# Performance work log

Measured on AMD Instinct MI355X. Metric: run time of the kernel, lower is better.

Reference implementation:

```python
import jax, jax.numpy as jnp
import numpy as np

DIM = 1024
NUM_HEADS = 16
HEAD_DIM = DIM // NUM_HEADS
SCALING = HEAD_DIM ** (-0.5)


def setup_inputs() -> dict:
    key = jax.random.key(0)
    ks = jax.random.split(key, 9)
    B, S = 2, 2048
    s = DIM ** -0.5  # ~ torch Linear init scale
    inp = {
        "x": jax.random.normal(ks[0], (B, S, DIM), dtype=jnp.float32),
        "wq": jax.random.uniform(ks[1], (DIM, DIM), jnp.float32, -s, s),
        "bq": jax.random.uniform(ks[2], (DIM,), jnp.float32, -s, s),
        "wk": jax.random.uniform(ks[3], (DIM, DIM), jnp.float32, -s, s),
        "bk": jax.random.uniform(ks[4], (DIM,), jnp.float32, -s, s),
        "wv": jax.random.uniform(ks[5], (DIM, DIM), jnp.float32, -s, s),
        "bv": jax.random.uniform(ks[6], (DIM,), jnp.float32, -s, s),
        "wo": jax.random.uniform(ks[7], (DIM, DIM), jnp.float32, -s, s),
        "bo": jax.random.uniform(ks[8], (DIM,), jnp.float32, -s, s),
    }
    return inp


def reference(x, wq, bq, wk, bk, wv, bv, wo, bo):
    B, S, D = x.shape
    # projections (weights stored [out,in] like torch Linear -> x @ W.T + b)
    q = (x @ wq.T + bq).reshape(B, S, NUM_HEADS, HEAD_DIM)
    k = (x @ wk.T + bk).reshape(B, S, NUM_HEADS, HEAD_DIM)
    v = (x @ wv.T + bv).reshape(B, S, NUM_HEADS, HEAD_DIM)
    # [B,H,S,S] scores, scaled
    scores = jnp.einsum("bqhd,bkhd->bhqk", q, k) * SCALING
    attn = jax.nn.softmax(scores, axis=-1)
    # dropout p=0.0 (eval): identity
    out = jnp.einsum("bhqk,bkhd->bqhd", attn, v).reshape(B, S, D)
    return out @ wo.T + bo
```

## Files before the change

kernel.cpp:

```cpp
#include <hip/hip_runtime.h>

#define DIM 1024
#define NHEADS 16
#define HDIM 64
#define BATCH 2
#define SEQ 2048
#define MTOT (BATCH*SEQ)
#define QSCALE 0.18033688011112042f
#define XN ((size_t)MTOT*DIM)
#define WN ((size_t)DIM*DIM)

typedef __attribute__((ext_vector_type(8))) short short8;
typedef __attribute__((ext_vector_type(4))) float f32x4;
typedef __attribute__((ext_vector_type(16))) float f32x16;
typedef __attribute__((ext_vector_type(2))) int int2v;

static __device__ __forceinline__ unsigned short bf16rne(float f) {
    unsigned u = __builtin_bit_cast(unsigned, f);
    return (unsigned short)((u + 0x7fffu + ((u >> 16) & 1u)) >> 16);
}

static __device__ __forceinline__ void gld16(const void* g, void* l) {
    __builtin_amdgcn_global_load_lds((const __attribute__((address_space(1))) void*)g,
                                     (__attribute__((address_space(3))) void*)l, 16, 0, 0);
}

static __device__ __forceinline__ f32x16 mfma32(short8 a, short8 b, f32x16 c) {
    return __builtin_amdgcn_mfma_f32_32x32x16_bf16(a, b, c, 0, 0, 0);
}

__global__ __launch_bounds__(256)
void prep(const float* __restrict__ x, const float* __restrict__ wq, const float* __restrict__ wk,
          const float* __restrict__ wv, const float* __restrict__ wo, unsigned short* __restrict__ dst)
{
    const size_t i = ((size_t)blockIdx.x*256 + threadIdx.x)*8;
    const float* s; size_t o;
    if (i < XN)           { s = x;  o = i; }
    else if (i < XN+WN)   { s = wq; o = i - XN; }
    else if (i < XN+2*WN) { s = wk; o = i - XN - WN; }
    else if (i < XN+3*WN) { s = wv; o = i - XN - 2*WN; }
    else                  { s = wo; o = i - XN - 3*WN; }
    float4 a = *(const float4*)(s + o);
    float4 b = *(const float4*)(s + o + 4);
    uint4 w;
    w.x = (unsigned)bf16rne(a.x) | ((unsigned)bf16rne(a.y) << 16);
    w.y = (unsigned)bf16rne(a.z) | ((unsigned)bf16rne(a.w) << 16);
    w.z = (unsigned)bf16rne(b.x) | ((unsigned)bf16rne(b.y) << 16);
    w.w = (unsigned)bf16rne(b.z) | ((unsigned)bf16rne(b.w) << 16);
    *(uint4*)&dst[i] = w;
}

__global__ __launch_bounds__(256)
void gemm_qkv(const unsigned short* __restrict__ A,
              const unsigned short* __restrict__ W0, const unsigned short* __restrict__ W1,
              const unsigned short* __restrict__ W2,
              const float* __restrict__ b0, const float* __restrict__ b1, const float* __restrict__ b2,
              unsigned short* __restrict__ o0, unsigned short* __restrict__ o1, unsigned short* __restrict__ o2)
{
    __shared__ __align__(16) unsigned short smem[24576];
    #define AS(s) (smem + (s)*4096)
    #define BS(s) (smem + 12288 + (s)*4096)
    const int t = threadIdx.x, wid = t >> 6, lane = t & 63;
    const int lr = lane & 15, lg = lane >> 4;
    const int bid = blockIdx.y * 24 + blockIdx.x;
    const int swz = (bid & 7) * 96 + (bid >> 3);
    const int sx = swz % 24, sy = swz / 24;
    const int widx = sx >> 3;
    const int n0 = (sx & 7) << 7;
    const int m0 = sy << 7;
    const unsigned short* W = widx == 0 ? W0 : (widx == 1 ? W1 : W2);
    const float* bias        = widx == 0 ? b0 : (widx == 1 ? b1 : b2);

    const int wm = wid >> 1, wn = wid & 1;
    const int f0 = 2*wid, f1 = f0 + 1;
    const unsigned short* Ag0 = A + (size_t)(m0 + f0*16 + lr)*DIM + lg*8;
    const unsigned short* Ag1 = A + (size_t)(m0 + f1*16 + lr)*DIM + lg*8;
    const unsigned short* Bg0 = W + (size_t)(n0 + f0*16 + lr)*DIM + lg*8;
    const unsigned short* Bg1 = W + (size_t)(n0 + f1*16 + lr)*DIM + lg*8;

    auto stage = [&](int tt, int slot) {
        const int ko = tt * 32;
        gld16(Ag0 + ko, AS(slot) + f0*512); gld16(Ag1 + ko, AS(slot) + f1*512);
        gld16(Bg0 + ko, BS(slot) + f0*512); gld16(Bg1 + ko, BS(slot) + f1*512);
    };

    f32x4 acc[4][4] = {};
    stage(0, 0); stage(1, 1);
    int c0 = 0, c1 = 1, c2 = 2;

    for (int it = 0; it < DIM/32; ++it) {
        if (it < DIM/32 - 2) { asm volatile("s_waitcnt vmcnt(4)" ::: "memory"); }
        else                 { asm volatile("s_waitcnt vmcnt(0)" ::: "memory"); }
        __builtin_amdgcn_s_barrier();
        short8 af[4], bf[4];
        #pragma unroll
        for (int i = 0; i < 4; ++i) af[i] = *(const short8*)(AS(c0) + (wm*4+i)*512 + lane*8);
        #pragma unroll
        for (int i = 0; i < 4; ++i) bf[i] = *(const short8*)(BS(c0) + (wn*4+i)*512 + lane*8);
        if (it + 2 < DIM/32) stage(it + 2, c2);
        __builtin_amdgcn_s_setprio(1);
        #pragma unroll
        for (int mb = 0; mb < 4; ++mb)
            #pragma unroll
            for (int nb = 0; nb < 4; ++nb)
                acc[mb][nb] = __builtin_amdgcn_mfma_f32_16x16x32_bf16(af[mb], bf[nb], acc[mb][nb], 0, 0, 0);
        __builtin_amdgcn_s_setprio(0);
        const int tmp = c0; c0 = c1; c1 = c2; c2 = tmp;
    }

    if (widx == 0) {
        #pragma unroll
        for (int nb = 0; nb < 4; ++nb) {
            const int col = n0 + wn*64 + nb*16 + lr;
            const float bv = bias[col];
            #pragma unroll
            for (int mb = 0; mb < 4; ++mb) {
                #pragma unroll
                for (int j = 0; j < 4; ++j) {
                    const int row = m0 + wm*64 + mb*16 + lg*4 + j;
                    o0[(size_t)row*DIM + col] = bf16rne((acc[mb][nb][j] + bv) * QSCALE);
                }
            }
        }
    } else {
        unsigned short* outp = (widx == 1) ? o1 : o2;
        const int isV = (widx == 2);
        __syncthreads();
        unsigned short (*tile)[136] = (unsigned short (*)[136])smem;
        #pragma unroll
        for (int nb = 0; nb < 4; ++nb) {
            const int col = wn*64 + nb*16 + lr;
            const float bv = bias[n0 + col];
            #pragma unroll
            for (int mb = 0; mb < 4; ++mb) {
                #pragma unroll
                for (int j = 0; j < 4; ++j)
                    tile[wm*64 + mb*16 + lg*4 + j][col] = bf16rne(acc[mb][nb][j] + bv);
            }
        }
        __syncthreads();
        const int bb  = m0 >> 11;
        const int kt0 = (m0 & (SEQ-1)) >> 6;
        const int hh0 = n0 >> 6;
        #pragma unroll
        for (int shot = 0; shot < 8; ++shot) {
            const int idx = t + shot*256;
            const int tid = idx >> 9;
            const int fr  = (idx >> 6) & 7;
            const int ln  = idx & 63;
            const int ktl = tid & 1, hhl = tid >> 1;
            short8 ov;
            if (isV) {
                const int r0 = ktl*64 + (fr & 3)*16 + (ln >> 5)*8;
                const int c  = hhl*64 + (fr >> 2)*32 + (ln & 31);
                #pragma unroll
                for (int e = 0; e < 8; ++e) ov[e] = (short)tile[r0 + e][c];
            } else {
                const int r  = ktl*64 + (fr >> 2)*32 + (ln & 31);
                const int cc = hhl*64 + (fr & 3)*16 + (ln >> 5)*8;
                ov = *(const short8*)&tile[r][cc];
            }
            unsigned short* dst = outp
                + ((size_t)((bb*NHEADS + hh0 + hhl)*32 + kt0 + ktl))*4096 + fr*512 + ln*8;
            *(short8*)dst = ov;
        }
    }
    #undef AS
    #undef BS
}

__global__ __launch_bounds__(256)
void gemm_o(const unsigned short* __restrict__ A, const unsigned short* __restrict__ W,
            const float* __restrict__ bias, float* __restrict__ fo)
{
    __shared__ __align__(16) unsigned short As[3][2048];
    __shared__ __align__(16) unsigned short Bs[3][4096];
    const int t = threadIdx.x, wid = t >> 6, lane = t & 63;
    const int lr = lane & 15, lg = lane >> 4;
    const int bid = blockIdx.y * 8 + blockIdx.x;
    const int swz = (bid & 7) * 64 + (bid >> 3);
    const int n0 = (swz & 7) << 7;
    const int m0 = (swz >> 3) << 6;
    const int wm = wid >> 1, wn = wid & 1;

    const int fa = wid;
    const int g0 = 2*wid, g1 = g0 + 1;
    const unsigned short* Ag  = A + (size_t)(m0 + fa*16 + lr)*DIM + lg*8;
    const unsigned short* Bg0 = W + (size_t)(n0 + g0*16 + lr)*DIM + lg*8;
    const unsigned short* Bg1 = W + (size_t)(n0 + g1*16 + lr)*DIM + lg*8;

    auto stage = [&](int tt, int slot) {
        const int ko = tt * 32;
        gld16(Ag + ko, &As[slot][fa*512]);
        gld16(Bg0 + ko, &Bs[slot][g0*512]); gld16(Bg1 + ko, &Bs[slot][g1*512]);
    };

    f32x4 acc[2][4] = {};
    stage(0, 0); stage(1, 1);
    int c0 = 0, c1 = 1, c2 = 2;

    for (int it = 0; it < DIM/32; ++it) {
        if (it < DIM/32 - 2) { asm volatile("s_waitcnt vmcnt(3)" ::: "memory"); }
        else                 { asm volatile("s_waitcnt vmcnt(0)" ::: "memory"); }
        __builtin_amdgcn_s_barrier();
        short8 af[2], bf[4];
        #pragma unroll
        for (int i = 0; i < 2; ++i) af[i] = *(const short8*)&As[c0][(wm*2+i)*512 + lane*8];
        #pragma unroll
        for (int i = 0; i < 4; ++i) bf[i] = *(const short8*)&Bs[c0][(wn*4+i)*512 + lane*8];
        if (it + 2 < DIM/32) stage(it + 2, c2);
        __builtin_amdgcn_s_setprio(1);
        #pragma unroll
        for (int mb = 0; mb < 2; ++mb)
            #pragma unroll
            for (int nb = 0; nb < 4; ++nb)
                acc[mb][nb] = __builtin_amdgcn_mfma_f32_16x16x32_bf16(af[mb], bf[nb], acc[mb][nb], 0, 0, 0);
        __builtin_amdgcn_s_setprio(0);
        const int tmp = c0; c0 = c1; c1 = c2; c2 = tmp;
    }

    #pragma unroll
    for (int nb = 0; nb < 4; ++nb) {
        const int col = n0 + wn*64 + nb*16 + lr;
        const float bv = bias[col];
        #pragma unroll
        for (int mb = 0; mb < 2; ++mb) {
            #pragma unroll
            for (int j = 0; j < 4; ++j) {
                const int row = m0 + wm*32 + mb*16 + lg*4 + j;
                fo[(size_t)row*DIM + col] = acc[mb][nb][j] + bv;
            }
        }
    }
}

struct PA { short8 p[4]; };

static __device__ __forceinline__ PA softmax_pack(const f32x16& s0, const f32x16& s1, float& lsum) {
    float rsum = 0.f;
    unsigned pw0[4][2], pw1[4][2];
    #pragma unroll
    for (int r1 = 0; r1 < 4; ++r1)
        #pragma unroll
        for (int tt = 0; tt < 2; ++tt) {
            float pa_ = __builtin_amdgcn_exp2f(s0[4*r1+2*tt]);
            float pb_ = __builtin_amdgcn_exp2f(s0[4*r1+2*tt+1]);
            float pc_ = __builtin_amdgcn_exp2f(s1[4*r1+2*tt]);
            float pd_ = __builtin_amdgcn_exp2f(s1[4*r1+2*tt+1]);
            rsum += (pa_ + pb_) + (pc_ + pd_);
            asm("v_cvt_pk_bf16_f32 %0, %1, %2" : "=v"(pw0[r1][tt]) : "v"(pa_), "v"(pb_));
            asm("v_cvt_pk_bf16_f32 %0, %1, %2" : "=v"(pw1[r1][tt]) : "v"(pc_), "v"(pd_));
        }
    rsum += __shfl_xor(rsum, 32);
    lsum += rsum;
    PA r;
    #pragma unroll
    for (int ss = 0; ss < 4; ++ss) {
        union { short8 s8; unsigned u[4]; } pu;
        #pragma unroll
        for (int tt = 0; tt < 2; ++tt) {
            const unsigned a = (ss >> 1) ? pw1[2*(ss&1)][tt]   : pw0[2*(ss&1)][tt];
            const unsigned b = (ss >> 1) ? pw1[2*(ss&1)+1][tt] : pw0[2*(ss&1)+1][tt];
            int2v sw = __builtin_amdgcn_permlane32_swap((int)a, (int)b, false, false);
            pu.u[tt]     = (unsigned)sw[0];
            pu.u[2 + tt] = (unsigned)sw[1];
        }
        r.p[ss] = pu.s8;
    }
    return r;
}

__global__ __launch_bounds__(256)
void attn_mfma2(const unsigned short* __restrict__ Q, const unsigned short* __restrict__ Kp,
                const unsigned short* __restrict__ Vp, unsigned short* __restrict__ O)
{
    __shared__ __align__(16) unsigned short Ks[4][4096];
    __shared__ __align__(16) unsigned short Vs[4][4096];
    const int t = threadIdx.x, wid = t >> 6, lane = t & 63;
    const int l31 = lane & 31, h = lane >> 5;
    const int bid = blockIdx.y * 16 + blockIdx.x;
    const int swz = (bid & 7) * 64 + (bid >> 3);
    const int qt = swz & 15, bh = swz >> 4;
    const int b = bh >> 4, hh = bh & 15;
    const size_t qkbase = (size_t)b*SEQ*DIM + (size_t)hh*HDIM;
    const unsigned short* Qb = Q + qkbase;
    unsigned short*       Ob = O + qkbase;
    const int q0 = qt*128 + wid*32;

    short8 qf[4];
    #pragma unroll
    for (int ds = 0; ds < 4; ++ds)
        qf[ds] = *(const short8*)&Qb[(size_t)(q0 + l31)*DIM + ds*16 + h*8];

    const int f0 = 2*wid, f1 = f0 + 1;
    const unsigned short* Kg0 = Kp + (size_t)bh*32*4096 + f0*512 + lane*8;
    const unsigned short* Kg1 = Kg0 + 512;
    const unsigned short* Vg0 = Vp + (size_t)bh*32*4096 + f0*512 + lane*8;
    const unsigned short* Vg1 = Vg0 + 512;

    auto stage = [&](int tn) {
        const size_t ko = (size_t)tn * 4096;
        const int bb = tn & 3;
        gld16(Kg0 + ko, &Ks[bb][f0*512]); gld16(Kg1 + ko, &Ks[bb][f1*512]);
        gld16(Vg0 + ko, &Vs[bb][f0*512]); gld16(Vg1 + ko, &Vs[bb][f1*512]);
    };

    f32x16 ctx0 = {}, ctx1 = {};
    float lsum = 0.0f;

    stage(0); stage(1);

    const int NW = SEQ/128;
    for (int w = 0; w < NW; ++w) {
        const int t0 = 2*w;
        const int ba = t0 & 3, bb2 = (t0+1) & 3;
        const bool more = (w + 1 < NW);

        if (more) { asm volatile("s_waitcnt vmcnt(4)" ::: "memory"); }
        else      { asm volatile("s_waitcnt vmcnt(0)" ::: "memory"); }
        __builtin_amdgcn_s_barrier();
        if (more) stage(t0 + 2);

        f32x16 s0a = {}, s1a = {};
        __builtin_amdgcn_s_setprio(1);
        #pragma unroll
        for (int ds = 0; ds < 4; ++ds) {
            short8 kf0 = *(const short8*)&Ks[ba][ds*512 + lane*8];
            short8 kf1 = *(const short8*)&Ks[ba][(4+ds)*512 + lane*8];
            s0a = mfma32(kf0, qf[ds], s0a);
            s1a = mfma32(kf1, qf[ds], s1a);
        }
        __builtin_amdgcn_s_setprio(0);

        PA pa = softmax_pack(s0a, s1a, lsum);

        if (more) { asm volatile("s_waitcnt vmcnt(4)" ::: "memory"); }
        else      { asm volatile("s_waitcnt vmcnt(0)" ::: "memory"); }
        __builtin_amdgcn_s_barrier();
        if (more) stage(t0 + 3);

        f32x16 s0b = {}, s1b = {};
        __builtin_amdgcn_s_setprio(1);
        #pragma unroll
        for (int ds = 0; ds < 4; ++ds) {
            short8 kf0 = *(const short8*)&Ks[bb2][ds*512 + lane*8];
            short8 kf1 = *(const short8*)&Ks[bb2][(4+ds)*512 + lane*8];
            s0b = mfma32(kf0, qf[ds], s0b);
            s1b = mfma32(kf1, qf[ds], s1b);
        }
        #pragma unroll
        for (int ss = 0; ss < 4; ++ss) {
            short8 vf0 = *(const short8*)&Vs[ba][ss*512 + lane*8];
            short8 vf1 = *(const short8*)&Vs[ba][(4+ss)*512 + lane*8];
            ctx0 = mfma32(pa.p[ss], vf0, ctx0);
            ctx1 = mfma32(pa.p[ss], vf1, ctx1);
        }
        __builtin_amdgcn_s_setprio(0);

        PA pb = softmax_pack(s0b, s1b, lsum);

        __builtin_amdgcn_s_setprio(1);
        #pragma unroll
        for (int ss = 0; ss < 4; ++ss) {
            short8 vf0 = *(const short8*)&Vs[bb2][ss*512 + lane*8];
            short8 vf1 = *(const short8*)&Vs[bb2][(4+ss)*512 + lane*8];
            ctx0 = mfma32(pb.p[ss], vf0, ctx0);
            ctx1 = mfma32(pb.p[ss], vf1, ctx1);
        }
        __builtin_amdgcn_s_setprio(0);
    }

    const float linv = 1.0f / lsum;
    #pragma unroll
    for (int r = 0; r < 16; ++r) {
        const int qrow = (r&3) + 8*(r>>2) + 4*h;
        const float nm = __shfl(linv, qrow);
        unsigned short* p = &Ob[(size_t)(q0 + qrow)*DIM + l31];
        p[0]  = bf16rne(ctx0[r] * nm);
        p[32] = bf16rne(ctx1[r] * nm);
    }
}

extern "C" void kernel_launch(void* const* d_in, const int* in_sizes, int n_in,
                              void* d_out, int out_size, void* d_ws, size_t ws_size,
                              hipStream_t stream) {
    const float* x  = (const float*)d_in[0];
    const float* wq = (const float*)d_in[1];
    const float* bq = (const float*)d_in[2];
    const float* wk = (const float*)d_in[3];
    const float* bk = (const float*)d_in[4];
    const float* wv = (const float*)d_in[5];
    const float* bv = (const float*)d_in[6];
    const float* wo = (const float*)d_in[7];
    const float* bo = (const float*)d_in[8];
    float* out = (float*)d_out;

    unsigned short* Xb  = (unsigned short*)d_ws;
    unsigned short* Wqb = Xb  + XN;
    unsigned short* Wkb = Wqb + WN;
    unsigned short* Wvb = Wkb + WN;
    unsigned short* Wob = Wvb + WN;
    unsigned short* Qb  = Wob + WN;
    unsigned short* Kpb = Qb  + XN;
    unsigned short* Vpb = Kpb + XN;
    unsigned short* Cb  = Xb;

    prep<<<4096, 256, 0, stream>>>(x, wq, wk, wv, wo, Xb);

    gemm_qkv<<<dim3(24, 32), 256, 0, stream>>>(Xb, Wqb, Wkb, Wvb, bq, bk, bv, Qb, Kpb, Vpb);

    attn_mfma2<<<dim3(SEQ/128, BATCH*NHEADS), 256, 0, stream>>>(Qb, Kpb, Vpb, Cb);

    gemm_o<<<dim3(8, 64), 256, 0, stream>>>(Cb, Wob, bo, out);
}
```

Measured before the change: 133.2 us.

## Process 64 query rows per wave in attention with 128-thread blocks

The attention kernel now runs 2 waves per block instead of 4, and each wave handles two 32-row query tiles, so every K and V fragment read from LDS feeds twice as many MFMAs. Staging per wave doubles to keep the same tile coverage, and the vmcnt thresholds are adjusted to match. The aim is less LDS read traffic per MFMA and fewer waves contending at barriers. The cost is many more accumulator registers, which can lower occupancy, and fewer waves per block to hide softmax latency.

Result: slower. 138.1 us (+3.7%).

```diff
diff --git a/kernel.cpp b/kernel.cpp
--- a/kernel.cpp
+++ b/kernel.cpp
@@ -270,7 +270,7 @@
     return r;
 }
 
-__global__ __launch_bounds__(256)
+__global__ __launch_bounds__(128)
 void attn_mfma2(const unsigned short* __restrict__ Q, const unsigned short* __restrict__ Kp,
                 const unsigned short* __restrict__ Vp, unsigned short* __restrict__ O)
 {
@@ -285,28 +285,30 @@
     const size_t qkbase = (size_t)b*SEQ*DIM + (size_t)hh*HDIM;
     const unsigned short* Qb = Q + qkbase;
     unsigned short*       Ob = O + qkbase;
-    const int q0 = qt*128 + wid*32;
-
-    short8 qf[4];
+    const int q0 = qt*128 + wid*64;
+
+    short8 qfA[4], qfB[4];
     #pragma unroll
-    for (int ds = 0; ds < 4; ++ds)
-        qf[ds] = *(const short8*)&Qb[(size_t)(q0 + l31)*DIM + ds*16 + h*8];
-
-    const int f0 = 2*wid, f1 = f0 + 1;
-    const unsigned short* Kg0 = Kp + (size_t)bh*32*4096 + f0*512 + lane*8;
-    const unsigned short* Kg1 = Kg0 + 512;
-    const unsigned short* Vg0 = Vp + (size_t)bh*32*4096 + f0*512 + lane*8;
-    const unsigned short* Vg1 = Vg0 + 512;
+    for (int ds = 0; ds < 4; ++ds) {
+        qfA[ds] = *(const short8*)&Qb[(size_t)(q0 + l31)*DIM + ds*16 + h*8];
+        qfB[ds] = *(const short8*)&Qb[(size_t)(q0 + 32 + l31)*DIM + ds*16 + h*8];
+    }
+
+    const unsigned short* Kg = Kp + (size_t)bh*32*4096 + 4*wid*512 + lane*8;
+    const unsigned short* Vg = Vp + (size_t)bh*32*4096 + 4*wid*512 + lane*8;
 
     auto stage = [&](int tn) {
         const size_t ko = (size_t)tn * 4096;
         const int bb = tn & 3;
-        gld16(Kg0 + ko, &Ks[bb][f0*512]); gld16(Kg1 + ko, &Ks[bb][f1*512]);
-        gld16(Vg0 + ko, &Vs[bb][f0*512]); gld16(Vg1 + ko, &Vs[bb][f1*512]);
+        #pragma unroll
+        for (int i = 0; i < 4; ++i) {
+            gld16(Kg + ko + i*512, &Ks[bb][(4*wid + i)*512]);
+            gld16(Vg + ko + i*512, &Vs[bb][(4*wid + i)*512]);
+        }
     };
 
-    f32x16 ctx0 = {}, ctx1 = {};
-    float lsum = 0.0f;
+    f32x16 ctxA0 = {}, ctxA1 = {}, ctxB0 = {}, ctxB1 = {};
+    float lsumA = 0.0f, lsumB = 0.0f;
 
     stage(0); stage(1);
 
@@ -316,68 +318,83 @@
         const int ba = t0 & 3, bb2 = (t0+1) & 3;
         const bool more = (w + 1 < NW);
 
-        if (more) { asm volatile("s_waitcnt vmcnt(4)" ::: "memory"); }
+        if (more) { asm volatile("s_waitcnt vmcnt(8)" ::: "memory"); }
         else      { asm volatile("s_waitcnt vmcnt(0)" ::: "memory"); }
         __builtin_amdgcn_s_barrier();
         if (more) stage(t0 + 2);
 
-        f32x16 s0a = {}, s1a = {};
+        f32x16 s0A = {}, s1A = {}, s0B = {}, s1B = {};
         __builtin_amdgcn_s_setprio(1);
         #pragma unroll
         for (int ds = 0; ds < 4; ++ds) {
             short8 kf0 = *(const short8*)&Ks[ba][ds*512 + lane*8];
             short8 kf1 = *(const short8*)&Ks[ba][(4+ds)*512 + lane*8];
-            s0a = mfma32(kf0, qf[ds], s0a);
-            s1a = mfma32(kf1, qf[ds], s1a);
+            s0A = mfma32(kf0, qfA[ds], s0A);
+            s1A = mfma32(kf1, qfA[ds], s1A);
+            s0B = mfma32(kf0, qfB[ds], s0B);
+            s1B = mfma32(kf1, qfB[ds], s1B);
         }
         __builtin_amdgcn_s_setprio(0);
 
-        PA pa = softmax_pack(s0a, s1a, lsum);
-
-        if (more) { asm volatile("s_waitcnt vmcnt(4)" ::: "memory"); }
+        PA paA = softmax_pack(s0A, s1A, lsumA);
+        PA paB = softmax_pack(s0B, s1B, lsumB);
+
+        if (more) { asm volatile("s_waitcnt vmcnt(8)" ::: "memory"); }
         else      { asm volatile("s_waitcnt vmcnt(0)" ::: "memory"); }
         __builtin_amdgcn_s_barrier();
         if (more) stage(t0 + 3);
 
-        f32x16 s0b = {}, s1b = {};
+        f32x16 r0A = {}, r1A = {}, r0B = {}, r1B = {};
         __builtin_amdgcn_s_setprio(1);
         #pragma unroll
         for (int ds = 0; ds < 4; ++ds) {
             short8 kf0 = *(const short8*)&Ks[bb2][ds*512 + lane*8];
             short8 kf1 = *(const short8*)&Ks[bb2][(4+ds)*512 + lane*8];
-            s0b = mfma32(kf0, qf[ds], s0b);
-            s1b = mfma32(kf1, qf[ds], s1b);
+            r0A = mfma32(kf0, qfA[ds], r0A);
+            r1A = mfma32(kf1, qfA[ds], r1A);
+            r0B = mfma32(kf0, qfB[ds], r0B);
+            r1B = mfma32(kf1, qfB[ds], r1B);
         }
         #pragma unroll
         for (int ss = 0; ss < 4; ++ss) {
             short8 vf0 = *(const short8*)&Vs[ba][ss*512 + lane*8];
             short8 vf1 = *(const short8*)&Vs[ba][(4+ss)*512 + lane*8];
-            ctx0 = mfma32(pa.p[ss], vf0, ctx0);
-            ctx1 = mfma32(pa.p[ss], vf1, ctx1);
+            ctxA0 = mfma32(paA.p[ss], vf0, ctxA0);
+            ctxA1 = mfma32(paA.p[ss], vf1, ctxA1);
+            ctxB0 = mfma32(paB.p[ss], vf0, ctxB0);
+            ctxB1 = mfma32(paB.p[ss], vf1, ctxB1);
         }
         __builtin_amdgcn_s_setprio(0);
 
-        PA pb = softmax_pack(s0b, s1b, lsum);
+        PA pbA = softmax_pack(r0A, r1A, lsumA);
+        PA pbB = softmax_pack(r0B, r1B, lsumB);
 
         __builtin_amdgcn_s_setprio(1);
         #pragma unroll
         for (int ss = 0; ss < 4; ++ss) {
             short8 vf0 = *(const short8*)&Vs[bb2][ss*512 + lane*8];
             short8 vf1 = *(const short8*)&Vs[bb2][(4+ss)*512 + lane*8];
-            ctx0 = mfma32(pb.p[ss], vf0, ctx0);
-            ctx1 = mfma32(pb.p[ss], vf1, ctx1);
+            ctxA0 = mfma32(pbA.p[ss], vf0, ctxA0);
+            ctxA1 = mfma32(pbA.p[ss], vf1, ctxA1);
+            ctxB0 = mfma32(pbB.p[ss], vf0, ctxB0);
+            ctxB1 = mfma32(pbB.p[ss], vf1, ctxB1);
         }
         __builtin_amdgcn_s_setprio(0);
     }
 
-    const float linv = 1.0f / lsum;
+    const float linvA = 1.0f / lsumA;
+    const float linvB = 1.0f / lsumB;
     #pragma unroll
     for (int r = 0; r < 16; ++r) {
         const int qrow = (r&3) + 8*(r>>2) + 4*h;
-        const float nm = __shfl(linv, qrow);
-        unsigned short* p = &Ob[(size_t)(q0 + qrow)*DIM + l31];
-        p[0]  = bf16rne(ctx0[r] * nm);
-        p[32] = bf16rne(ctx1[r] * nm);
+        const float nmA = __shfl(linvA, qrow);
+        const float nmB = __shfl(linvB, qrow);
+        unsigned short* pA = &Ob[(size_t)(q0 + qrow)*DIM + l31];
+        unsigned short* pB = &Ob[(size_t)(q0 + 32 + qrow)*DIM + l31];
+        pA[0]  = bf16rne(ctxA0[r] * nmA);
+        pA[32] = bf16rne(ctxA1[r] * nmA);
+        pB[0]  = bf16rne(ctxB0[r] * nmB);
+        pB[32] = bf16rne(ctxB1[r] * nmB);
     }
 }
 
@@ -409,7 +426,7 @@
 
     gemm_qkv<<<dim3(24, 32), 256, 0, stream>>>(Xb, Wqb, Wkb, Wvb, bq, bk, bv, Qb, Kpb, Vpb);
 
-    attn_mfma2<<<dim3(SEQ/128, BATCH*NHEADS), 256, 0, stream>>>(Qb, Kpb, Vpb, Cb);
+    attn_mfma2<<<dim3(16, BATCH*NHEADS), 128, 0, stream>>>(Qb, Kpb, Vpb, Cb);
 
     gemm_o<<<dim3(8, 64), 256, 0, stream>>>(Cb, Wob, bo, out);
 }
```
